# Optimization experiments

Hardware: AMD Instinct MI355X
Metric: run time of the kernel (lower is better)

## Reference

```python
import jax, jax.numpy as jnp
import numpy as np
import math

HID, HEADS, HD = 1024, 16, 64
DFF = 4 * HID
EPS = 1e-6
RES_SCALE = 0.5

def build_alibi_slopes(n_heads):
    def get_slopes(power):
        start = 2 ** (-2 ** (-(math.log2(power) - 3)))
        return [start * start ** i for i in range(power)]
    if math.log2(n_heads).is_integer():
        slopes = get_slopes(n_heads)
    else:
        closest = 2 ** math.floor(math.log2(n_heads))
        slopes = get_slopes(closest)
        extra = get_slopes(2 * closest)
        slopes = slopes + extra[0::2][: n_heads - closest]
    return jnp.asarray(np.array(slopes, dtype=np.float32))

def rmsnorm(x, w):
    var = jnp.mean(x * x, axis=-1, keepdims=True)
    return x * jax.lax.rsqrt(var + EPS) * w

def setup_inputs() -> dict:
    key = jax.random.key(0)
    ks = jax.random.split(key, 12)
    s = lambda d: 1.0 / math.sqrt(d)
    return {
        "x": jax.random.normal(ks[0], (2, 2048, HID), dtype=jnp.float32),
        "norm1_w": jnp.ones((HID,), jnp.float32),
        "Wq": jax.random.normal(ks[1], (HID, HEADS * HD), jnp.float32) * s(HID),
        "bq": jax.random.normal(ks[2], (HEADS * HD,), jnp.float32) * 0.01,
        "Wk": jax.random.normal(ks[3], (HID, HEADS * HD), jnp.float32) * s(HID),
        "bk": jax.random.normal(ks[4], (HEADS * HD,), jnp.float32) * 0.01,
        "Wv": jax.random.normal(ks[5], (HID, HEADS * HD), jnp.float32) * s(HID),
        "Wo": jax.random.normal(ks[6], (HEADS * HD, HID), jnp.float32) * s(HEADS * HD),
        "norm2_w": jnp.ones((HID,), jnp.float32),
        "W1": jax.random.normal(ks[7], (HID, DFF), jnp.float32) * s(HID),
        "b1": jax.random.normal(ks[8], (DFF,), jnp.float32) * 0.01,
        "W2": jax.random.normal(ks[9], (DFF, HID), jnp.float32) * s(DFF),
        "b2": jax.random.normal(ks[10], (HID,), jnp.float32) * 0.01,
    }

def reference(x, norm1_w, Wq, bq, Wk, bk, Wv, Wo, norm2_w, W1, b1, W2, b2):
    b, s, _ = x.shape
    scale = HD ** -0.5
    xn = rmsnorm(x, norm1_w)
    q = (xn @ Wq + bq).reshape(b, s, HEADS, HD).transpose(0, 2, 1, 3)
    k = (xn @ Wk + bk).reshape(b, s, HEADS, HD).transpose(0, 2, 1, 3)
    v = (xn @ Wv).reshape(b, s, HEADS, HD).transpose(0, 2, 1, 3)
    scores = jnp.einsum('bhqd,bhkd->bhqk', q, k) * scale
    pos = jnp.arange(s)
    dist = jnp.abs(pos[None, :] - pos[:, None]).astype(scores.dtype)  # [s,s]
    slopes = build_alibi_slopes(HEADS)
    bias = -slopes[:, None, None] * dist[None, :, :]  # [h,s,s]
    scores = scores + bias[None]
    weights = jax.nn.softmax(scores, axis=-1)
    attn = jnp.einsum('bhqk,bhkd->bhqd', weights, v)
    attn = attn.transpose(0, 2, 1, 3).reshape(b, s, HEADS * HD)
    x = x + attn @ Wo
    xn2 = rmsnorm(x, norm2_w)
    h = jax.nn.gelu(xn2 @ W1 + b1, approximate=False)
    x = x + RES_SCALE * (h @ W2 + b2)
    return x
```

## Files before the change

### kernel.cpp

```cpp
#include <hip/hip_runtime.h>
#include <hip/hip_bf16.h>
#include <math.h>

#define S_LEN   2048
#define HIDN    1024
#define NHEADS  16
#define HDIM    64
#define NTOK    4096
#define DFFN    4096

#define LOG2E 1.44269504088896f

typedef __attribute__((ext_vector_type(8))) __bf16 bf16x8;
typedef __attribute__((ext_vector_type(4))) float  f32x4;

static __device__ __forceinline__ ushort f2bf(float f) {
  union { float f; unsigned u; } v; v.f = f;
  unsigned u = v.u;
  unsigned r = (u + 0x7fffu + ((u >> 16) & 1u)) >> 16;
  return (ushort)r;
}

#define GLOAD16(gp, lp)                                                              \
  __builtin_amdgcn_global_load_lds((const __attribute__((address_space(1))) void*)(gp), \
                                   (__attribute__((address_space(3))) void*)(lp), 16, 0, 0)

__global__ __launch_bounds__(256) void convert_wT(const float* __restrict__ W,
                                                  ushort* __restrict__ WT,
                                                  int K, int N) {
  __shared__ float tile[32][33];
  int n0 = blockIdx.x * 32, k0 = blockIdx.y * 32;
  int tx = threadIdx.x & 31, ty = threadIdx.x >> 5;
#pragma unroll
  for (int i = 0; i < 4; i++)
    tile[ty + i * 8][tx] = W[(size_t)(k0 + ty + i * 8) * N + n0 + tx];
  __syncthreads();
#pragma unroll
  for (int i = 0; i < 4; i++)
    WT[(size_t)(n0 + ty + i * 8) * K + k0 + tx] = f2bf(tile[tx][ty + i * 8]);
}

__global__ void build_bias(const float* __restrict__ bq, const float* __restrict__ bk,
                           float* __restrict__ biasqkv) {
  int i = blockIdx.x * 256 + threadIdx.x;
  if (i < 3 * HIDN) {
    float v = (i < HIDN) ? bq[i] : (i < 2 * HIDN ? bk[i - HIDN] : 0.0f);
    biasqkv[i] = v;
  }
}

__global__ __launch_bounds__(256) void rmsnorm_kernel(const float* __restrict__ x,
                                                      const float* __restrict__ w,
                                                      ushort* __restrict__ out) {
  int row = blockIdx.x, t = threadIdx.x;
  const float4* x4 = (const float4*)(x + (size_t)row * HIDN);
  float4 v = x4[t];
  float ss = v.x * v.x + v.y * v.y + v.z * v.z + v.w * v.w;
#pragma unroll
  for (int m = 32; m; m >>= 1) ss += __shfl_xor(ss, m, 64);
  __shared__ float wsum[4];
  if ((t & 63) == 0) wsum[t >> 6] = ss;
  __syncthreads();
  float tot = wsum[0] + wsum[1] + wsum[2] + wsum[3];
  float rs = rsqrtf(tot * (1.0f / HIDN) + 1e-6f);
  const float4* w4 = (const float4*)w;
  float4 wv = w4[t];
  ushort4 o;
  o.x = f2bf(v.x * rs * wv.x);
  o.y = f2bf(v.y * rs * wv.y);
  o.z = f2bf(v.z * rs * wv.z);
  o.w = f2bf(v.w * rs * wv.w);
  *(ushort4*)(out + (size_t)row * HIDN + t * 4) = o;
}

template <int EPI, int TM>
__global__ __launch_bounds__(256, 3) void gemm_bt(const ushort* __restrict__ A,
                                                  const ushort* __restrict__ B,
                                                  int M, int N, int K,
                                                  const float* __restrict__ bias,
                                                  const float* __restrict__ resid,
                                                  float* __restrict__ outf,
                                                  ushort* __restrict__ outb,
                                                  ushort* __restrict__ qb,
                                                  ushort* __restrict__ kb,
                                                  ushort* __restrict__ vb) {
  constexpr int NF  = (TM == 128) ? 4 : 2;
  constexpr int ACH = TM / 64;
  __shared__ __align__(16) ushort As[TM * 32];
  __shared__ __align__(16) ushort Bs[128 * 32];
  int t = threadIdx.x;
  int w = t >> 6, l = t & 63;
  int wmr = (TM == 128) ? (w >> 1) * 64 : 0;
  int wnc = (TM == 128) ? (w & 1) * 64 : w * 32;
  int lr = l & 15, lg = l >> 4, g8 = lg * 8;
  int m0 = blockIdx.x * TM, n0 = blockIdx.y * 128;

  int scol = (l & 3) * 8;
  const ushort* Ag = A + (size_t)(m0 + w * 16 * ACH + (l >> 2)) * K + scol;
  const ushort* Bg = B + (size_t)(n0 + w * 32 + (l >> 2)) * K + scol;
  ushort* Asw = &As[(w * 16 * ACH) * 32];
  ushort* Bsw = &Bs[(w * 32) * 32];

  f32x4 acc[4][NF] = {};

  for (int k0 = 0; k0 < K; k0 += 32) {
    GLOAD16(Ag + k0, Asw);
    if constexpr (ACH == 2) GLOAD16(Ag + (size_t)16 * K + k0, Asw + 16 * 32);
    GLOAD16(Bg + k0, Bsw);
    GLOAD16(Bg + (size_t)16 * K + k0, Bsw + 16 * 32);
    __syncthreads();

    bf16x8 af[4], bfr[NF];
#pragma unroll
    for (int mf = 0; mf < 4; mf++)
      af[mf] = *(const bf16x8*)(&As[(wmr + mf * 16 + lr) * 32 + g8]);
#pragma unroll
    for (int nf = 0; nf < NF; nf++)
      bfr[nf] = *(const bf16x8*)(&Bs[(wnc + nf * 16 + lr) * 32 + g8]);
#pragma unroll
    for (int mf = 0; mf < 4; mf++)
#pragma unroll
      for (int nf = 0; nf < NF; nf++)
        acc[mf][nf] = __builtin_amdgcn_mfma_f32_16x16x32_bf16(af[mf], bfr[nf], acc[mf][nf], 0, 0, 0);
    __syncthreads();
  }

  if constexpr (EPI == 0) {
#pragma unroll
    for (int mf = 0; mf < 4; mf++) {
      int row0 = m0 + wmr + mf * 16 + lg * 4;
      int bb = row0 >> 11, ss0 = row0 & 2047;
#pragma unroll
      for (int nf = 0; nf < NF; nf++) {
        int col = n0 + wnc + nf * 16 + lr;
        float bcol = bias[col];
        int which = col >> 10, nn = col & 1023;
        int hh = nn >> 6, dd = nn & 63;
        if (which == 2) {
          ushort4 o;
          o.x = f2bf(acc[mf][nf][0] + bcol);
          o.y = f2bf(acc[mf][nf][1] + bcol);
          o.z = f2bf(acc[mf][nf][2] + bcol);
          o.w = f2bf(acc[mf][nf][3] + bcol);
          *(ushort4*)(vb + ((size_t)(bb * NHEADS + hh) * HDIM + dd) * S_LEN + ss0) = o;
        } else {
#pragma unroll
          for (int r = 0; r < 4; r++) {
            float v = acc[mf][nf][r] + bcol;
            size_t idx = ((size_t)(bb * NHEADS + hh) * S_LEN + ss0 + r) * HDIM + dd;
            if (which == 0) qb[idx] = f2bf(v * (0.125f * LOG2E));
            else kb[idx] = f2bf(v);
          }
        }
      }
    }
  } else {
#pragma unroll
    for (int mf = 0; mf < 4; mf++) {
#pragma unroll
      for (int nf = 0; nf < NF; nf++) {
#pragma unroll
        for (int r = 0; r < 4; r++) {
          int row = m0 + wmr + mf * 16 + lg * 4 + r;
          int col = n0 + wnc + nf * 16 + lr;
          float v = acc[mf][nf][r];
          if constexpr (EPI == 1) {
            outf[(size_t)row * HIDN + col] = resid[(size_t)row * HIDN + col] + v;
          } else if constexpr (EPI == 2) {
            float tv = v + bias[col];
            float gl = 0.5f * tv * (1.0f + erff(tv * 0.70710678118f));
            outb[(size_t)row * DFFN + col] = f2bf(gl);
          } else {
            outf[(size_t)row * HIDN + col] =
                resid[(size_t)row * HIDN + col] + 0.5f * (v + bias[col]);
          }
        }
      }
    }
  }
}

__global__ __launch_bounds__(256, 2) void attn_kernel(const ushort* __restrict__ qb,
                                                      const ushort* __restrict__ kb,
                                                      const ushort* __restrict__ vt,
                                                      ushort* __restrict__ attn_out) {
  __shared__ __align__(16) ushort Ks[2][64 * 64];
  __shared__ __align__(16) ushort VTs[2][64 * 64];
  __shared__ __align__(16) ushort Ps[4][16 * 72];
  int t = threadIdx.x;
  int w = t >> 6, l = t & 63;
  int lr = l & 15, lg = l >> 4, g8 = lg * 8;
  int blk = blockIdx.x;
  int qt = blk & 31;
  int bh = blk >> 5;
  int h = bh & 15;
  float slope2 = exp2f(-0.5f * (float)(h + 1)) * LOG2E;
  int q0 = qt * 64;
  const ushort* qp = qb + (size_t)bh * S_LEN * HDIM;

  int srow = w * 16 + (l >> 3);
  int sgr  = ((l & 7) ^ (l >> 3)) * 8;
  const ushort* kbase = kb + (size_t)bh * S_LEN * HDIM + (size_t)srow * HDIM + sgr;
  const ushort* vbase = vt + (size_t)bh * HDIM * S_LEN + (size_t)srow * S_LEN + sgr;

  auto stage = [&](int tile, int b) {
    const ushort* ksrc = kbase + (size_t)tile * 64 * HDIM;
    const ushort* vsrc = vbase + tile * 64;
    GLOAD16(ksrc,                       &Ks[b][(w * 16) * 64]);
    GLOAD16(ksrc + 8 * HDIM,            &Ks[b][(w * 16 + 8) * 64]);
    GLOAD16(vsrc,                       &VTs[b][(w * 16) * 64]);
    GLOAD16(vsrc + (size_t)8 * S_LEN,   &VTs[b][(w * 16 + 8) * 64]);
  };

  bf16x8 qf[2];
#pragma unroll
  for (int ks = 0; ks < 2; ks++)
    qf[ks] = *(const bf16x8*)(qp + (size_t)(q0 + w * 16 + lr) * HDIM + ks * 32 + g8);

  float qpf[4];
#pragma unroll
  for (int r = 0; r < 4; r++) qpf[r] = (float)(q0 + w * 16 + lg * 4 + r);

  f32x4 ao[4] = {};
  float mrow[4] = {-INFINITY, -INFINITY, -INFINITY, -INFINITY};
  float lden[4] = {0.f, 0.f, 0.f, 0.f};

  stage(0, 0);
  __syncthreads();

  for (int tt = 0; tt < S_LEN / 64; tt++) {
    int cur = tt & 1;
    if (tt + 1 < S_LEN / 64) stage(tt + 1, cur ^ 1);

    f32x4 sc[4];
#pragma unroll
    for (int nf = 0; nf < 4; nf++) {
      f32x4 a = {};
#pragma unroll
      for (int ks = 0; ks < 2; ks++) {
        bf16x8 kf = *(const bf16x8*)(&Ks[cur][(nf * 16 + lr) * 64 +
                                             (((ks * 4 + lg) ^ (lr & 7)) << 3)]);
        a = __builtin_amdgcn_mfma_f32_16x16x32_bf16(qf[ks], kf, a, 0, 0, 0);
      }
      sc[nf] = a;
    }

    float pmax[4];
#pragma unroll
    for (int r = 0; r < 4; r++) {
      float mx = -INFINITY;
#pragma unroll
      for (int nf = 0; nf < 4; nf++) {
        float kpos = (float)(tt * 64 + nf * 16 + lr);
        float s = sc[nf][r] - slope2 * fabsf(qpf[r] - kpos);
        sc[nf][r] = s;
        mx = fmaxf(mx, s);
      }
#pragma unroll
      for (int m = 1; m < 16; m <<= 1) mx = fmaxf(mx, __shfl_xor(mx, m, 64));
      pmax[r] = mx;
    }

    int need = 0;
#pragma unroll
    for (int r = 0; r < 4; r++) need |= (pmax[r] > mrow[r]);
    if (__any(need)) {
#pragma unroll
      for (int r = 0; r < 4; r++) {
        float mn = fmaxf(mrow[r], pmax[r]);
        float scl = exp2f(mrow[r] - mn);
        mrow[r] = mn;
        lden[r] *= scl;
#pragma unroll
        for (int nf = 0; nf < 4; nf++) ao[nf][r] *= scl;
      }
    }

#pragma unroll
    for (int r = 0; r < 4; r++) {
      float su = 0.f;
#pragma unroll
      for (int nf = 0; nf < 4; nf++) {
        float p = exp2f(sc[nf][r] - mrow[r]);
        sc[nf][r] = p;
        su += p;
      }
#pragma unroll
      for (int m = 1; m < 16; m <<= 1) su += __shfl_xor(su, m, 64);
      lden[r] += su;
    }
#pragma unroll
    for (int nf = 0; nf < 4; nf++)
#pragma unroll
      for (int r = 0; r < 4; r++)
        Ps[w][(lg * 4 + r) * 72 + nf * 16 + lr] = f2bf(sc[nf][r]);
    asm volatile("s_waitcnt lgkmcnt(0)" ::: "memory");
    __builtin_amdgcn_sched_barrier(0);

    bf16x8 pf[2];
#pragma unroll
    for (int ks = 0; ks < 2; ks++)
      pf[ks] = *(const bf16x8*)(&Ps[w][lr * 72 + ks * 32 + g8]);
#pragma unroll
    for (int nf = 0; nf < 4; nf++) {
#pragma unroll
      for (int ks = 0; ks < 2; ks++) {
        bf16x8 vf = *(const bf16x8*)(&VTs[cur][(nf * 16 + lr) * 64 +
                                              (((ks * 4 + lg) ^ (lr & 7)) << 3)]);
        ao[nf] = __builtin_amdgcn_mfma_f32_16x16x32_bf16(pf[ks], vf, ao[nf], 0, 0, 0);
      }
    }
    __syncthreads();
  }

  int token_base = (bh >> 4) * S_LEN + q0 + w * 16;
#pragma unroll
  for (int nf = 0; nf < 4; nf++) {
#pragma unroll
    for (int r = 0; r < 4; r++) {
      int token = token_base + lg * 4 + r;
      int d = nf * 16 + lr;
      attn_out[(size_t)token * HIDN + h * HDIM + d] = f2bf(ao[nf][r] / lden[r]);
    }
  }
}

extern "C" void kernel_launch(void* const* d_in, const int* in_sizes, int n_in,
                              void* d_out, int out_size, void* d_ws, size_t ws_size,
                              hipStream_t stream) {
  const float* x   = (const float*)d_in[0];
  const float* n1w = (const float*)d_in[1];
  const float* Wq  = (const float*)d_in[2];
  const float* bq  = (const float*)d_in[3];
  const float* Wk  = (const float*)d_in[4];
  const float* bk  = (const float*)d_in[5];
  const float* Wv  = (const float*)d_in[6];
  const float* Wo  = (const float*)d_in[7];
  const float* n2w = (const float*)d_in[8];
  const float* W1  = (const float*)d_in[9];
  const float* b1  = (const float*)d_in[10];
  const float* W2  = (const float*)d_in[11];
  const float* b2  = (const float*)d_in[12];
  float* out = (float*)d_out;

  char* ws = (char*)d_ws;
  ushort* xn     = (ushort*)(ws + 0);
  ushort* wqkvT  = (ushort*)(ws + 8388608);
  ushort* woT    = (ushort*)(ws + 14680064);
  ushort* w1T    = (ushort*)(ws + 16777216);
  ushort* w2T    = (ushort*)(ws + 25165824);
  float*  biasq  = (float*)(ws + 33554432);
  ushort* qbuf   = (ushort*)(ws + 33566720);
  ushort* kbuf   = (ushort*)(ws + 41955328);
  ushort* vtbuf  = (ushort*)(ws + 50343936);
  ushort* attnb  = (ushort*)(ws + 58732544);
  float*  x2     = (float*)(ws + 67121152);
  ushort* xn2    = (ushort*)(ws + 83898368);
  ushort* hbuf   = qbuf;

  dim3 blk(256);

  convert_wT<<<dim3(32, 32), blk, 0, stream>>>(Wq, wqkvT, HIDN, HIDN);
  convert_wT<<<dim3(32, 32), blk, 0, stream>>>(Wk, wqkvT + 1024 * 1024, HIDN, HIDN);
  convert_wT<<<dim3(32, 32), blk, 0, stream>>>(Wv, wqkvT + 2 * 1024 * 1024, HIDN, HIDN);
  convert_wT<<<dim3(32, 32), blk, 0, stream>>>(Wo, woT, HIDN, HIDN);
  convert_wT<<<dim3(128, 32), blk, 0, stream>>>(W1, w1T, HIDN, DFFN);
  convert_wT<<<dim3(32, 128), blk, 0, stream>>>(W2, w2T, DFFN, HIDN);
  build_bias<<<12, blk, 0, stream>>>(bq, bk, biasq);

  rmsnorm_kernel<<<NTOK, blk, 0, stream>>>(x, n1w, xn);
  gemm_bt<0, 128><<<dim3(32, 24), blk, 0, stream>>>(xn, wqkvT, NTOK, 3 * HIDN, HIDN,
                                                    biasq, nullptr, nullptr, nullptr,
                                                    qbuf, kbuf, vtbuf);
  attn_kernel<<<dim3(32 * 32), blk, 0, stream>>>(qbuf, kbuf, vtbuf, attnb);
  gemm_bt<1, 64><<<dim3(64, 8), blk, 0, stream>>>(attnb, woT, NTOK, HIDN, HIDN,
                                                  nullptr, x, x2, nullptr,
                                                  nullptr, nullptr, nullptr);
  rmsnorm_kernel<<<NTOK, blk, 0, stream>>>(x2, n2w, xn2);
  gemm_bt<2, 128><<<dim3(32, 32), blk, 0, stream>>>(xn2, w1T, NTOK, DFFN, HIDN,
                                                    b1, nullptr, nullptr, hbuf,
                                                    nullptr, nullptr, nullptr);
  gemm_bt<3, 64><<<dim3(64, 8), blk, 0, stream>>>(hbuf, w2T, NTOK, HIDN, DFFN,
                                                  b2, x2, out, nullptr,
                                                  nullptr, nullptr, nullptr);
}
```

Baseline: 455.6 us.

## Deepen GEMM K-tile to 64 with swizzled LDS and precompute ALiBi bias in attention

The GEMM kernel now stages 64-wide K slices with an XOR-swizzled LDS layout and issues two MFMAs per fragment pair per iteration. This halves the number of loop iterations and barriers and avoids LDS bank conflicts. The attention kernel seeds the QK accumulator with an incrementally updated ALiBi bias instead of computing abs distances per element, and handles only the diagonal tile specially. It also uses a cheaper round-half-up bf16 conversion for P and raises the occupancy hint to 3. The trade-offs are larger LDS and register pressure, and the accumulated bias may drift in float precision.

```diff
diff --git a/kernel.cpp b/kernel.cpp
--- a/kernel.cpp
+++ b/kernel.cpp
@@ -19,6 +19,10 @@
   unsigned u = v.u;
   unsigned r = (u + 0x7fffu + ((u >> 16) & 1u)) >> 16;
   return (ushort)r;
+}
+static __device__ __forceinline__ ushort f2bf_fast(float f) {
+  union { float f; unsigned u; } v; v.f = f;
+  return (ushort)((v.u + 0x8000u) >> 16);
 }
 
 #define GLOAD16(gp, lp)                                                              \
@@ -84,51 +88,62 @@
                                                   ushort* __restrict__ qb,
                                                   ushort* __restrict__ kb,
                                                   ushort* __restrict__ vb) {
-  constexpr int NF  = (TM == 128) ? 4 : 2;
-  constexpr int ACH = TM / 64;
-  __shared__ __align__(16) ushort As[TM * 32];
-  __shared__ __align__(16) ushort Bs[128 * 32];
+  constexpr int NF = (TM == 128) ? 4 : 2;
+  __shared__ __align__(16) ushort As[TM * 64];
+  __shared__ __align__(16) ushort Bs[128 * 64];
   int t = threadIdx.x;
   int w = t >> 6, l = t & 63;
   int wmr = (TM == 128) ? (w >> 1) * 64 : 0;
   int wnc = (TM == 128) ? (w & 1) * 64 : w * 32;
-  int lr = l & 15, lg = l >> 4, g8 = lg * 8;
+  int lr = l & 15, lg = l >> 4;
   int m0 = blockIdx.x * TM, n0 = blockIdx.y * 128;
 
-  int scol = (l & 3) * 8;
-  const ushort* Ag = A + (size_t)(m0 + w * 16 * ACH + (l >> 2)) * K + scol;
-  const ushort* Bg = B + (size_t)(n0 + w * 32 + (l >> 2)) * K + scol;
-  ushort* Asw = &As[(w * 16 * ACH) * 32];
-  ushort* Bsw = &Bs[(w * 32) * 32];
+  int srl = l >> 3;
+  int sg  = ((l & 7) ^ srl) * 8;
+  const ushort* Ag = A + (size_t)(m0 + w * (TM / 4) + srl) * K + sg;
+  const ushort* Bg = B + (size_t)(n0 + w * 32 + srl) * K + sg;
+  ushort* Asw = &As[(w * (TM / 4)) * 64];
+  ushort* Bsw = &Bs[(w * 32) * 64];
 
   f32x4 acc[4][NF] = {};
 
-  for (int k0 = 0; k0 < K; k0 += 32) {
-    GLOAD16(Ag + k0, Asw);
-    if constexpr (ACH == 2) GLOAD16(Ag + (size_t)16 * K + k0, Asw + 16 * 32);
-    GLOAD16(Bg + k0, Bsw);
-    GLOAD16(Bg + (size_t)16 * K + k0, Bsw + 16 * 32);
+  for (int k0 = 0; k0 < K; k0 += 64) {
+#pragma unroll
+    for (int c = 0; c < TM / 32; c++)
+      GLOAD16(Ag + (size_t)(8 * c) * K + k0, Asw + (8 * c) * 64);
+#pragma unroll
+    for (int c = 0; c < 4; c++)
+      GLOAD16(Bg + (size_t)(8 * c) * K + k0, Bsw + (8 * c) * 64);
     __syncthreads();
 
-    bf16x8 af[4], bfr[NF];
+    bf16x8 af[4][2], bfr[NF][2];
 #pragma unroll
     for (int mf = 0; mf < 4; mf++)
-      af[mf] = *(const bf16x8*)(&As[(wmr + mf * 16 + lr) * 32 + g8]);
+#pragma unroll
+      for (int ks = 0; ks < 2; ks++)
+        af[mf][ks] = *(const bf16x8*)(&As[(wmr + mf * 16 + lr) * 64 +
+                                          (((ks * 4 + lg) ^ (lr & 7)) << 3)]);
 #pragma unroll
     for (int nf = 0; nf < NF; nf++)
-      bfr[nf] = *(const bf16x8*)(&Bs[(wnc + nf * 16 + lr) * 32 + g8]);
+#pragma unroll
+      for (int ks = 0; ks < 2; ks++)
+        bfr[nf][ks] = *(const bf16x8*)(&Bs[(wnc + nf * 16 + lr) * 64 +
+                                           (((ks * 4 + lg) ^ (lr & 7)) << 3)]);
 #pragma unroll
     for (int mf = 0; mf < 4; mf++)
 #pragma unroll
-      for (int nf = 0; nf < NF; nf++)
-        acc[mf][nf] = __builtin_amdgcn_mfma_f32_16x16x32_bf16(af[mf], bfr[nf], acc[mf][nf], 0, 0, 0);
+      for (int nf = 0; nf < NF; nf++) {
+        acc[mf][nf] = __builtin_amdgcn_mfma_f32_16x16x32_bf16(af[mf][0], bfr[nf][0], acc[mf][nf], 0, 0, 0);
+        acc[mf][nf] = __builtin_amdgcn_mfma_f32_16x16x32_bf16(af[mf][1], bfr[nf][1], acc[mf][nf], 0, 0, 0);
+      }
     __syncthreads();
   }
 
+  int lg4 = lg * 4;
   if constexpr (EPI == 0) {
 #pragma unroll
     for (int mf = 0; mf < 4; mf++) {
-      int row0 = m0 + wmr + mf * 16 + lg * 4;
+      int row0 = m0 + wmr + mf * 16 + lg4;
       int bb = row0 >> 11, ss0 = row0 & 2047;
 #pragma unroll
       for (int nf = 0; nf < NF; nf++) {
@@ -161,7 +176,7 @@
       for (int nf = 0; nf < NF; nf++) {
 #pragma unroll
         for (int r = 0; r < 4; r++) {
-          int row = m0 + wmr + mf * 16 + lg * 4 + r;
+          int row = m0 + wmr + mf * 16 + lg4 + r;
           int col = n0 + wnc + nf * 16 + lr;
           float v = acc[mf][nf][r];
           if constexpr (EPI == 1) {
@@ -180,7 +195,7 @@
   }
 }
 
-__global__ __launch_bounds__(256, 2) void attn_kernel(const ushort* __restrict__ qb,
+__global__ __launch_bounds__(256, 3) void attn_kernel(const ushort* __restrict__ qb,
                                                       const ushort* __restrict__ kb,
                                                       const ushort* __restrict__ vt,
                                                       ushort* __restrict__ attn_out) {
@@ -195,6 +210,7 @@
   int bh = blk >> 5;
   int h = bh & 15;
   float slope2 = exp2f(-0.5f * (float)(h + 1)) * LOG2E;
+  float s64 = slope2 * 64.0f;
   int q0 = qt * 64;
   const ushort* qp = qb + (size_t)bh * S_LEN * HDIM;
 
@@ -217,14 +233,19 @@
   for (int ks = 0; ks < 2; ks++)
     qf[ks] = *(const bf16x8*)(qp + (size_t)(q0 + w * 16 + lr) * HDIM + ks * 32 + g8);
 
-  float qpf[4];
-#pragma unroll
-  for (int r = 0; r < 4; r++) qpf[r] = (float)(q0 + w * 16 + lg * 4 + r);
-
   f32x4 ao[4] = {};
   float mrow[4] = {-INFINITY, -INFINITY, -INFINITY, -INFINITY};
   float lden[4] = {0.f, 0.f, 0.f, 0.f};
 
+  f32x4 biasv[4];
+  if (qt > 0) {
+#pragma unroll
+    for (int nf = 0; nf < 4; nf++)
+#pragma unroll
+      for (int r = 0; r < 4; r++)
+        biasv[nf][r] = -slope2 * (float)(q0 + w * 16 + lg * 4 + r - nf * 16 - lr);
+  }
+
   stage(0, 0);
   __syncthreads();
 
@@ -232,10 +253,12 @@
     int cur = tt & 1;
     if (tt + 1 < S_LEN / 64) stage(tt + 1, cur ^ 1);
 
+    bool diag = (tt == qt);
+
     f32x4 sc[4];
 #pragma unroll
     for (int nf = 0; nf < 4; nf++) {
-      f32x4 a = {};
+      f32x4 a = diag ? f32x4{0.f, 0.f, 0.f, 0.f} : biasv[nf];
 #pragma unroll
       for (int ks = 0; ks < 2; ks++) {
         bf16x8 kf = *(const bf16x8*)(&Ks[cur][(nf * 16 + lr) * 64 +
@@ -245,17 +268,27 @@
       sc[nf] = a;
     }
 
+    if (diag) {
+#pragma unroll
+      for (int nf = 0; nf < 4; nf++) {
+        float kk = (float)(nf * 16 + lr);
+#pragma unroll
+        for (int r = 0; r < 4; r++) {
+          float qq = (float)(w * 16 + lg * 4 + r);
+          sc[nf][r] -= slope2 * fabsf(qq - kk);
+        }
+      }
+#pragma unroll
+      for (int nf = 0; nf < 4; nf++)
+#pragma unroll
+        for (int r = 0; r < 4; r++)
+          biasv[nf][r] = -slope2 * (float)(64 + nf * 16 + lr - w * 16 - lg * 4 - r);
+    }
+
     float pmax[4];
 #pragma unroll
     for (int r = 0; r < 4; r++) {
-      float mx = -INFINITY;
-#pragma unroll
-      for (int nf = 0; nf < 4; nf++) {
-        float kpos = (float)(tt * 64 + nf * 16 + lr);
-        float s = sc[nf][r] - slope2 * fabsf(qpf[r] - kpos);
-        sc[nf][r] = s;
-        mx = fmaxf(mx, s);
-      }
+      float mx = fmaxf(fmaxf(sc[0][r], sc[1][r]), fmaxf(sc[2][r], sc[3][r]));
 #pragma unroll
       for (int m = 1; m < 16; m <<= 1) mx = fmaxf(mx, __shfl_xor(mx, m, 64));
       pmax[r] = mx;
@@ -293,7 +326,7 @@
     for (int nf = 0; nf < 4; nf++)
 #pragma unroll
       for (int r = 0; r < 4; r++)
-        Ps[w][(lg * 4 + r) * 72 + nf * 16 + lr] = f2bf(sc[nf][r]);
+        Ps[w][(lg * 4 + r) * 72 + nf * 16 + lr] = f2bf_fast(sc[nf][r]);
     asm volatile("s_waitcnt lgkmcnt(0)" ::: "memory");
     __builtin_amdgcn_sched_barrier(0);
 
@@ -309,6 +342,15 @@
                                               (((ks * 4 + lg) ^ (lr & 7)) << 3)]);
         ao[nf] = __builtin_amdgcn_mfma_f32_16x16x32_bf16(pf[ks], vf, ao[nf], 0, 0, 0);
       }
+    }
+
+    int next = tt + 1;
+    if (!diag && next != qt) {
+      float d = (next < qt) ? s64 : -s64;
+#pragma unroll
+      for (int nf = 0; nf < 4; nf++)
+#pragma unroll
+        for (int r = 0; r < 4; r++) biasv[nf][r] += d;
     }
     __syncthreads();
   }
```

Measured after the change: 453.2 us. About the same (-0.5%).
